# Performance work log

Measured on AMD Instinct MI355X. Metric: run time of the kernel, lower is better.

Reference implementation:

```python
import jax, jax.numpy as jnp
import numpy as np

N = 256          # waveguide_dims
ITERN = 3        # iter_num
B = 8192         # batch
INDEX_END = 10   # MNIST classes
ALPHA = 0.1
G = 0.05 * np.pi
PHI_B = np.pi


def setup_inputs() -> dict:
    key = jax.random.key(0)
    k1, k2, k3, k4, k5 = jax.random.split(key, 5)
    two_pi = 2.0 * np.pi
    return {
        "x_real": jax.random.normal(k1, (B, N), dtype=jnp.float32),
        "x_imag": jax.random.normal(k2, (B, N), dtype=jnp.float32),
        "theta": jax.random.uniform(k3, (ITERN, N, N // 2), dtype=jnp.float32) * two_pi,
        "phi":   jax.random.uniform(k4, (ITERN, N, N // 2), dtype=jnp.float32) * two_pi,
        "gamma": jax.random.uniform(k5, (ITERN, N), dtype=jnp.float32) * two_pi,
    }


def _mzi_mesh(x, theta, phi, gamma):
    """Rectangular (Clements) MZI mesh: N layers of 2x2 rotations + output phases.
    x: [B, N] complex64; theta, phi: [N, N//2]; gamma: [N]."""
    L = theta.shape[0]
    shifts = jnp.arange(L) % 2                      # even/odd layer offset
    full = jnp.ones((N // 2,), dtype=bool)
    odd = full.at[-1].set(False)                    # wrap-around pair inactive on odd layers
    masks = jnp.where((shifts == 1)[:, None], odd[None, :], full[None, :])

    def step(xc, inp):
        th, ph, sh, mk = inp
        xr = jnp.roll(xc, -sh, axis=1).reshape(-1, N // 2, 2)
        x0, x1 = xr[..., 0], xr[..., 1]
        half = 0.5 * th
        s, c = jnp.sin(half), jnp.cos(half)
        pre = 1j * jnp.exp(1j * half)               # common MZI prefactor
        ep = jnp.exp(1j * ph)
        y0 = pre * (ep * s * x0 + c * x1)
        y1 = pre * (ep * c * x0 - s * x1)
        y0 = jnp.where(mk, y0, x0)
        y1 = jnp.where(mk, y1, x1)
        y = jnp.stack([y0, y1], axis=-1).reshape(-1, N)
        return jnp.roll(y, sh, axis=1), None

    x, _ = jax.lax.scan(step, x, (theta, phi, shifts, masks))
    return x * jnp.exp(1j * gamma)[None, :]


def _eo_nonlin(x):
    # phase = 0.5*g*|x|^2 + 0.5*phi_b ; out = sqrt(1-alpha)*cos(phase)*exp(-i phase)*x
    phase = 0.5 * G * (x.real ** 2 + x.imag ** 2) + 0.5 * PHI_B
    return np.float32(np.sqrt(1.0 - ALPHA)) * jnp.cos(phase) * jnp.exp(-1j * phase) * x


def reference(x_real, x_imag, theta, phi, gamma):
    x = x_real.astype(jnp.complex64) + 1j * x_imag.astype(jnp.complex64)
    for i in range(ITERN):
        x = _mzi_mesh(x, theta[i], phi[i], gamma[i])
        if i != ITERN - 1:
            x = _eo_nonlin(x)
    intensity = x.real ** 2 + x.imag ** 2            # cnormsq
    norm = jnp.sqrt(jnp.sum(intensity ** 2, axis=1, keepdims=True))
    intensity = intensity / jnp.maximum(norm, 1e-12)  # F.normalize(dim=1)
    return intensity[:, :INDEX_END]
```

## Files before the change

### kernel.cpp

```cpp
#include <hip/hip_runtime.h>
#include <math.h>

#define NWG 256
#define NPAIR 128
#define NITER 3
#define NBATCH 8192
#define KDIM 512
#define MSZ (512*512)

typedef __attribute__((ext_vector_type(8))) short short8;
typedef __attribute__((ext_vector_type(8))) unsigned short ushort8v;
typedef __attribute__((ext_vector_type(4))) float floatx4;

static __device__ __forceinline__ unsigned short f2bf(float f) {
    unsigned int u = __float_as_uint(f);
    unsigned int r = (u + 0x7fffu + ((u >> 16) & 1u)) >> 16;
    return (unsigned short)r;
}
static __device__ __forceinline__ float bf2f(unsigned short h) {
    return __uint_as_float(((unsigned int)h) << 16);
}
static __device__ __forceinline__ void bsplit(float v, unsigned short &h, unsigned short &l) {
    h = f2bf(v);
    l = f2bf(v - bf2f(h));
}
static __device__ __forceinline__ void async16(const void* g, void* l) {
    __builtin_amdgcn_global_load_lds(
        (const __attribute__((address_space(1))) unsigned int*)g,
        (__attribute__((address_space(3))) unsigned int*)l, 16, 0, 0);
}

static __device__ __forceinline__ void apply2(
    float &x0r, float &x0i, float &x1r, float &x1i,
    const float4 a, const float4 b)
{
    float y0r = a.x*x0r - a.y*x0i + a.z*x1r - a.w*x1i;
    float y0i = a.x*x0i + a.y*x0r + a.z*x1i + a.w*x1r;
    float y1r = b.x*x0r - b.y*x0i + b.z*x1r - b.w*x1i;
    float y1i = b.x*x0i + b.y*x0r + b.z*x1i + b.w*x1r;
    x0r = y0r; x0i = y0i; x1r = y1r; x1i = y1i;
}

__global__ void precompute_kernel(const float* __restrict__ theta,
                                  const float* __restrict__ phi,
                                  const float* __restrict__ gamma,
                                  float* __restrict__ coef,
                                  float* __restrict__ coefT,
                                  float* __restrict__ gexp)
{
    int idx = blockIdx.x * blockDim.x + threadIdx.x;
    if (idx < NITER * NWG * NPAIR) {
        float h  = 0.5f * theta[idx];
        float ph = phi[idx];
        float sh = sinf(h),  ch = cosf(h);
        float sp = sinf(ph), cp = cosf(ph);
        float pr = -sh, pii = ch;
        float qr = pr*cp - pii*sp;
        float qi = pr*sp + pii*cp;
        float Ar = qr*sh,  Ai = qi*sh;
        float Br = pr*ch,  Bi = pii*ch;
        float Cr = qr*ch,  Ci = qi*ch;
        float Dr = -pr*sh, Di = -pii*sh;
        float4* o = (float4*)coef + (size_t)idx * 2;
        o[0] = make_float4(Ar,Ai,Br,Bi);
        o[1] = make_float4(Cr,Ci,Dr,Di);
        float4* ot = (float4*)coefT + (size_t)idx * 2;
        ot[0] = make_float4(Ar,Ai,Cr,Ci);
        ot[1] = make_float4(Br,Bi,Dr,Di);
    }
    if (idx < NITER * NWG) {
        float g = gamma[idx];
        gexp[idx*2]   = cosf(g);
        gexp[idx*2+1] = sinf(g);
    }
}

static __device__ __forceinline__ void store_row(
    unsigned short* __restrict__ bh, unsigned short* __restrict__ bl,
    int row, int lane, bool cj, const float xr[4], const float xi[4])
{
    ushort4 reH, reL, imH, imL, nimH, nimL;
    unsigned short h, l;
#pragma unroll
    for (int e = 0; e < 4; ++e) {
        bsplit(xr[e], h, l);  ((unsigned short*)&reH)[e]  = h; ((unsigned short*)&reL)[e]  = l;
        bsplit(xi[e], h, l);  ((unsigned short*)&imH)[e]  = h; ((unsigned short*)&imL)[e]  = l;
        bsplit(-xi[e], h, l); ((unsigned short*)&nimH)[e] = h; ((unsigned short*)&nimL)[e] = l;
    }
    ushort4 urH = cj ? imH : nimH, urL = cj ? imL : nimL;
    ushort4 llH = cj ? nimH : imH, llL = cj ? nimL : imL;
    *(ushort4*)(bh + (size_t)row*KDIM + 4*lane)             = reH;
    *(ushort4*)(bh + (size_t)row*KDIM + 256 + 4*lane)       = urH;
    *(ushort4*)(bh + (size_t)(row+256)*KDIM + 4*lane)       = llH;
    *(ushort4*)(bh + (size_t)(row+256)*KDIM + 256 + 4*lane) = reH;
    *(ushort4*)(bl + (size_t)row*KDIM + 4*lane)             = reL;
    *(ushort4*)(bl + (size_t)row*KDIM + 256 + 4*lane)       = urL;
    *(ushort4*)(bl + (size_t)(row+256)*KDIM + 4*lane)       = llL;
    *(ushort4*)(bl + (size_t)(row+256)*KDIM + 256 + 4*lane) = reL;
}

static __device__ __forceinline__ void layer_compute2(
    const float4 cc[4], int lane, int sp,
    float ar[4], float ai[4], float br[4], float bi[4])
{
    const float4 c0a = cc[0], c0b = cc[1], c1a = cc[2], c1b = cc[3];
    if ((sp & 1) == 0) {
        apply2(ar[0], ai[0], ar[1], ai[1], c0a, c0b);
        apply2(ar[2], ai[2], ar[3], ai[3], c1a, c1b);
        apply2(br[0], bi[0], br[1], bi[1], c0a, c0b);
        apply2(br[2], bi[2], br[3], bi[3], c1a, c1b);
    } else {
        float tAr = __shfl_down(ar[0], 1, 64);
        float tAi = __shfl_down(ai[0], 1, 64);
        float tBr = __shfl_down(br[0], 1, 64);
        float tBi = __shfl_down(bi[0], 1, 64);
        apply2(ar[1], ai[1], ar[2], ai[2], c0a, c0b);
        apply2(br[1], bi[1], br[2], bi[2], c0a, c0b);
        float x3r = ar[3], x3i = ai[3];
        float y3r = c1a.x*x3r - c1a.y*x3i + c1a.z*tAr - c1a.w*tAi;
        float y3i = c1a.x*x3i + c1a.y*x3r + c1a.z*tAi + c1a.w*tAr;
        float ynr = c1b.x*x3r - c1b.y*x3i + c1b.z*tAr - c1b.w*tAi;
        float yni = c1b.x*x3i + c1b.y*x3r + c1b.z*tAi + c1b.w*tAr;
        float w3r = br[3], w3i = bi[3];
        float z3r = c1a.x*w3r - c1a.y*w3i + c1a.z*tBr - c1a.w*tBi;
        float z3i = c1a.x*w3i + c1a.y*w3r + c1a.z*tBi + c1a.w*tBr;
        float znr = c1b.x*w3r - c1b.y*w3i + c1b.z*tBr - c1b.w*tBi;
        float zni = c1b.x*w3i + c1b.y*w3r + c1b.z*tBi + c1b.w*tBr;
        float rAr = __shfl_up(ynr, 1, 64);
        float rAi = __shfl_up(yni, 1, 64);
        float rBr = __shfl_up(znr, 1, 64);
        float rBi = __shfl_up(zni, 1, 64);
        if (lane != 63) { ar[3] = y3r; ai[3] = y3i; br[3] = z3r; bi[3] = z3i; }
        if (lane != 0)  { ar[0] = rAr; ai[0] = rAi; br[0] = rBr; bi[0] = rBi; }
    }
}

__global__ void propagate_kernel(const float* __restrict__ coef,
                                 const float* __restrict__ coefT,
                                 const float* __restrict__ gexp,
                                 unsigned short* __restrict__ chunkH,
                                 unsigned short* __restrict__ chunkL)
{
    __shared__ __align__(16) char smem[3 * 16384];

    const int tid  = threadIdx.x;
    const int lane = tid & 63;
    const int wv   = tid >> 6;
    const int grp  = blockIdx.x >> 6;
    const int it   = grp >> 2, c = grp & 3;
    const int r0   = (blockIdx.x & 63) * 4 + wv * 2;
    const int r1   = r0 + 1;
    const bool rev = (c & 1);
    const bool cj  = (c == 1) || (c == 2);

    float ar[4], ai[4], br[4], bi[4];
    float gc0 = 1.0f, gs0 = 0.0f, gc1 = 1.0f, gs1 = 0.0f;
    if (c == 3) {
        gc0 = gexp[(it*NWG + r0)*2]; gs0 = gexp[(it*NWG + r0)*2 + 1];
        gc1 = gexp[(it*NWG + r1)*2]; gs1 = gexp[(it*NWG + r1)*2 + 1];
    }
#pragma unroll
    for (int e = 0; e < 4; ++e) {
        bool on0 = (4*lane + e) == r0;
        bool on1 = (4*lane + e) == r1;
        ar[e] = on0 ? gc0 : 0.0f;  ai[e] = on0 ? gs0 : 0.0f;
        br[e] = on1 ? gc1 : 0.0f;  bi[e] = on1 ? gs1 : 0.0f;
    }

    const char* cbb = (const char*)(rev ? coefT : coef)
                    + (size_t)(it*NWG + c*64) * (NPAIR * 32);
    const int slot16 = (tid ^ ((tid >> 3) & 3)) * 16;

    auto stage = [&](int m) {
        char* dst = smem + (m % 3) * 16384;
#pragma unroll
        for (int q = 0; q < 4; ++q) {
            int s = 4*m + q;
            int r = rev ? 63 - s : s;
            const char* srow = cbb + (size_t)r * 4096;
            async16(srow + slot16,        dst + q*4096 + tid*16);
            async16(srow + slot16 + 2048, dst + q*4096 + tid*16 + 2048);
        }
    };

    stage(0); stage(1);

    const int sw = (lane >> 1) & 3;
    for (int m = 0; m < 16; ++m) {
        if (m < 15) asm volatile("s_waitcnt vmcnt(8)" ::: "memory");
        else        asm volatile("s_waitcnt vmcnt(0)" ::: "memory");
        __builtin_amdgcn_s_barrier();
        asm volatile("" ::: "memory");
        if (m < 14) stage(m + 2);
        const char* B = smem + (m % 3) * 16384;

        float4 cc[4][4];
#pragma unroll
        for (int q = 0; q < 4; ++q) {
            const char* Bq = B + q*4096;
            cc[q][0] = *(const float4*)(Bq + 16*(4*lane + (0 ^ sw)));
            cc[q][1] = *(const float4*)(Bq + 16*(4*lane + (1 ^ sw)));
            cc[q][2] = *(const float4*)(Bq + 16*(4*lane + (2 ^ sw)));
            cc[q][3] = *(const float4*)(Bq + 16*(4*lane + (3 ^ sw)));
        }
#pragma unroll
        for (int q = 0; q < 4; ++q) {
            int s = 4*m + q;
            layer_compute2(cc[q], lane, rev ? 63 - s : s, ar, ai, br, bi);
        }
    }

    unsigned short* bh = chunkH + (size_t)grp * MSZ;
    unsigned short* bl = chunkL + (size_t)grp * MSZ;
    store_row(bh, bl, r0, lane, cj, ar, ai);
    store_row(bh, bl, r1, lane, cj, br, bi);
}

__global__ __launch_bounds__(256, 2) void compose_kernel(
    const unsigned short* __restrict__ srcH, const unsigned short* __restrict__ srcL,
    unsigned short* __restrict__ outH, unsigned short* __restrict__ outL,
    unsigned short* __restrict__ bmat, int mode)
{
    __shared__ unsigned short sAh[3][2048], sAl[3][2048], sBh[3][2048], sBl[3][2048];
    const int z = blockIdx.z;
    const unsigned short *Ah, *Al, *Bh, *Bl;
    if (mode == 0) {
        int it = z >> 1, wh = z & 1;
        int ai = it*4 + (wh ? 3 : 0), bi = it*4 + (wh ? 2 : 1);
        Ah = srcH + (size_t)ai*MSZ; Al = srcL + (size_t)ai*MSZ;
        Bh = srcH + (size_t)bi*MSZ; Bl = srcL + (size_t)bi*MSZ;
    } else {
        Ah = srcH + (size_t)(2*z+1)*MSZ; Al = srcL + (size_t)(2*z+1)*MSZ;
        Bh = srcH + (size_t)(2*z)*MSZ;   Bl = srcL + (size_t)(2*z)*MSZ;
    }
    const int tid = threadIdx.x, lane = tid & 63, wv = tid >> 6;
    const int quad = lane >> 4, l16 = lane & 15;
    const int m0 = blockIdx.x * 64, n0 = blockIdx.y * 64;
    const unsigned short* src = (wv==0)?Ah:(wv==1)?Al:(wv==2)?Bh:Bl;
    unsigned short (*dstb)[2048] = (wv==0)?sAh:(wv==1)?sAl:(wv==2)?sBh:sBl;
    const int r0 = (wv < 2) ? m0 : n0;
    const int trowb = lane >> 2, tcol = (lane & 3) * 8;

    const unsigned short* sp[4];
#pragma unroll
    for (int i = 0; i < 4; ++i)
        sp[i] = src + (size_t)(r0 + i*16 + trowb)*KDIM + tcol;

    auto stage = [&](int s) {
        int kt = s * 32, bs = s % 3;
#pragma unroll
        for (int i = 0; i < 4; ++i)
            async16(sp[i] + kt, &dstb[bs][i*512 + lane*8]);
    };
    stage(0); stage(1);

    floatx4 acc[4] = {};
    for (int s = 0; s < 16; ++s) {
        if (s < 15) asm volatile("s_waitcnt vmcnt(4)" ::: "memory");
        else        asm volatile("s_waitcnt vmcnt(0)" ::: "memory");
        __builtin_amdgcn_s_barrier();
        asm volatile("" ::: "memory");
        if (s < 14) stage(s + 2);
        const int bs = s % 3;
        short8 ah = *(const short8*)&sAh[bs][(16*wv + l16)*32 + quad*8];
        short8 al = *(const short8*)&sAl[bs][(16*wv + l16)*32 + quad*8];
#pragma unroll
        for (int ni = 0; ni < 4; ++ni) {
            short8 bh = *(const short8*)&sBh[bs][(16*ni + l16)*32 + quad*8];
            short8 bl = *(const short8*)&sBl[bs][(16*ni + l16)*32 + quad*8];
            acc[ni] = __builtin_amdgcn_mfma_f32_16x16x32_bf16(ah, bh, acc[ni], 0,0,0);
            acc[ni] = __builtin_amdgcn_mfma_f32_16x16x32_bf16(ah, bl, acc[ni], 0,0,0);
            acc[ni] = __builtin_amdgcn_mfma_f32_16x16x32_bf16(al, bh, acc[ni], 0,0,0);
        }
    }
#pragma unroll
    for (int ni = 0; ni < 4; ++ni)
#pragma unroll
        for (int rg = 0; rg < 4; ++rg) {
            int r = m0 + 16*wv + quad*4 + rg;
            int cc = n0 + 16*ni + l16;
            float v = acc[ni][rg];
            if (mode == 0) {
                float vs = (((z & 1) == 0) && ((r >= 256) != (cc >= 256))) ? -v : v;
                unsigned short h, l; bsplit(vs, h, l);
                outH[(size_t)z*MSZ + (size_t)r*KDIM + cc] = h;
                outL[(size_t)z*MSZ + (size_t)r*KDIM + cc] = l;
            } else {
                bmat[(size_t)z*MSZ + (size_t)r*KDIM + cc] = f2bf(v);
            }
        }
}

__global__ void convert_kernel(const float* __restrict__ xre,
                               const float* __restrict__ xim,
                               unsigned short* __restrict__ xb)
{
    int idx = blockIdx.x * 256 + threadIdx.x;
    int b = idx >> 5, j = (idx & 31) << 3;
    const float* rp = xre + (size_t)b * 256 + j;
    const float* ip = xim + (size_t)b * 256 + j;
    float4 r0 = *(const float4*)rp, r1 = *(const float4*)(rp + 4);
    float4 i0 = *(const float4*)ip, i1 = *(const float4*)(ip + 4);
    ushort8v re, im;
    re[0]=f2bf(r0.x); re[1]=f2bf(r0.y); re[2]=f2bf(r0.z); re[3]=f2bf(r0.w);
    re[4]=f2bf(r1.x); re[5]=f2bf(r1.y); re[6]=f2bf(r1.z); re[7]=f2bf(r1.w);
    im[0]=f2bf(i0.x); im[1]=f2bf(i0.y); im[2]=f2bf(i0.z); im[3]=f2bf(i0.w);
    im[4]=f2bf(i1.x); im[5]=f2bf(i1.y); im[6]=f2bf(i1.z); im[7]=f2bf(i1.w);
    *(ushort8v*)(xb + (size_t)b * KDIM + j)       = re;
    *(ushort8v*)(xb + (size_t)b * KDIM + 256 + j) = im;
}

__global__ __launch_bounds__(256, 2) void gemm_kernel(
    const unsigned short* __restrict__ A, const unsigned short* __restrict__ Bm,
    int mode, unsigned short* __restrict__ xout, float* __restrict__ Iout)
{
    __shared__ unsigned short sA[3][64*32];
    __shared__ unsigned short sB[3][128*32];
    const int tid = threadIdx.x, lane = tid & 63, wv = tid >> 6;
    const int quad = lane >> 4, l16 = lane & 15;
    const int m0 = blockIdx.x * 64, n0 = blockIdx.y * 64;
    const int trowb = lane >> 2, tcol = (lane & 3) * 8;

    const unsigned short* srcA = A + (size_t)(m0 + 16*wv + trowb)*KDIM + tcol;
    int trow0 = 32*wv + trowb,  trow1 = 32*wv + 16 + trowb;
    int grow0 = (trow0 < 64) ? (n0 + trow0) : (n0 + trow0 + 192);
    int grow1 = (trow1 < 64) ? (n0 + trow1) : (n0 + trow1 + 192);
    const unsigned short* srcB0 = Bm + (size_t)grow0*KDIM + tcol;
    const unsigned short* srcB1 = Bm + (size_t)grow1*KDIM + tcol;

    auto stage = [&](int s) {
        int kt = s * 32, bs = s % 3;
        async16(srcA  + kt, &sA[bs][wv*512 + lane*8]);
        async16(srcB0 + kt, &sB[bs][(32*wv)*32 + lane*8]);
        async16(srcB1 + kt, &sB[bs][(32*wv + 16)*32 + lane*8]);
    };
    stage(0); stage(1);

    floatx4 acc[8] = {};
    for (int s = 0; s < 16; ++s) {
        if (s < 15) asm volatile("s_waitcnt vmcnt(3)" ::: "memory");
        else        asm volatile("s_waitcnt vmcnt(0)" ::: "memory");
        __builtin_amdgcn_s_barrier();
        asm volatile("" ::: "memory");
        if (s < 14) stage(s + 2);
        const int bs = s % 3;
        short8 a = *(const short8*)&sA[bs][(16*wv + l16)*32 + quad*8];
#pragma unroll
        for (int ni = 0; ni < 8; ++ni) {
            short8 b = *(const short8*)&sB[bs][(16*ni + l16)*32 + quad*8];
            acc[ni] = __builtin_amdgcn_mfma_f32_16x16x32_bf16(a, b, acc[ni], 0,0,0);
        }
    }
#pragma unroll
    for (int ni = 0; ni < 4; ++ni)
#pragma unroll
        for (int rg = 0; rg < 4; ++rg) {
            int row = m0 + 16*wv + quad*4 + rg;
            int cc  = n0 + 16*ni + l16;
            float yr = acc[ni][rg], yi = acc[ni+4][rg];
            if (mode == 2) {
                Iout[(size_t)row*256 + cc] = yr*yr + yi*yi;
            } else {
                float I = yr*yr + yi*yi;
                float phase = 0.078539816339744831f * I + 1.5707963267948966f;
                float sp, cp; __sincosf(phase, &sp, &cp);
                float f = 0.94868329805051381f * cp;
                xout[(size_t)row*KDIM + cc]       = f2bf(f*(cp*yr + sp*yi));
                xout[(size_t)row*KDIM + cc + 256] = f2bf(f*(cp*yi - sp*yr));
            }
        }
}

__global__ void final_kernel(const float* __restrict__ Ibuf,
                             float* __restrict__ out)
{
    const int lane = threadIdx.x & 63;
    const int wv   = threadIdx.x >> 6;
    const int row  = blockIdx.x * 4 + wv;
    float4 v = *(const float4*)(Ibuf + (size_t)row * 256 + 4*lane);
    float ss = v.x*v.x + v.y*v.y + v.z*v.z + v.w*v.w;
#pragma unroll
    for (int d = 1; d < 64; d <<= 1) ss += __shfl_xor(ss, d, 64);
    float inv = 1.0f / fmaxf(sqrtf(ss), 1e-12f);
    float* o = out + (size_t)row * 10;
    if (lane == 0)      { o[0]=v.x*inv; o[1]=v.y*inv; o[2]=v.z*inv; o[3]=v.w*inv; }
    else if (lane == 1) { o[4]=v.x*inv; o[5]=v.y*inv; o[6]=v.z*inv; o[7]=v.w*inv; }
    else if (lane == 2) { o[8]=v.x*inv; o[9]=v.y*inv; }
}

extern "C" void kernel_launch(void* const* d_in, const int* in_sizes, int n_in,
                              void* d_out, int out_size, void* d_ws, size_t ws_size,
                              hipStream_t stream)
{
    const float* x_real = (const float*)d_in[0];
    const float* x_imag = (const float*)d_in[1];
    const float* theta  = (const float*)d_in[2];
    const float* phi    = (const float*)d_in[3];
    const float* gamma  = (const float*)d_in[4];

    char* ws = (char*)d_ws;
    float* coef  = (float*)(ws + 0);
    float* coefT = (float*)(ws + 3145728);
    float* gexp  = (float*)(ws + 6291456);
    unsigned short* chunkH = (unsigned short*)(ws + 6297600);
    unsigned short* chunkL = (unsigned short*)(ws + 12589056);
    unsigned short* PH   = (unsigned short*)(ws + 0);
    unsigned short* PL   = (unsigned short*)(ws + 3145728);
    unsigned short* xbuf0 = (unsigned short*)(ws + 6297600);
    unsigned short* xbuf1 = (unsigned short*)(ws + 14686208);
    float* Ibuf = (float*)(ws + 14686208);
    unsigned short* Bmat = (unsigned short*)(ws + 23074816);

    precompute_kernel<<<(NITER*NWG*NPAIR + 255)/256, 256, 0, stream>>>(
        theta, phi, gamma, coef, coefT, gexp);

    propagate_kernel<<<768, 128, 0, stream>>>(coef, coefT, gexp, chunkH, chunkL);

    compose_kernel<<<dim3(8,8,6), 256, 0, stream>>>(chunkH, chunkL, PH, PL, Bmat, 0);
    compose_kernel<<<dim3(8,8,3), 256, 0, stream>>>(PH, PL, PH, PL, Bmat, 1);

    convert_kernel<<<NBATCH*NWG/8/256, 256, 0, stream>>>(x_real, x_imag, xbuf0);

    gemm_kernel<<<dim3(128,4), 256, 0, stream>>>(xbuf0, Bmat,           0, xbuf1, (float*)nullptr);
    gemm_kernel<<<dim3(128,4), 256, 0, stream>>>(xbuf1, Bmat + MSZ,     1, xbuf0, (float*)nullptr);
    gemm_kernel<<<dim3(128,4), 256, 0, stream>>>(xbuf0, Bmat + 2*MSZ,   2, (unsigned short*)nullptr, Ibuf);

    final_kernel<<<NBATCH/4, 256, 0, stream>>>(Ibuf, (float*)d_out);
}
```

Measured before the change: 169.2 us.

## Fuse fp32-to-bf16 input conversion into first GEMM and deepen K-stage

Removes the separate convert kernel: the first GEMM now loads fp32 real/imag inputs directly into registers, converts them to bf16 and writes them to shared memory in a 3-deep software pipeline. The other GEMM modes now stage 64-wide K tiles (two 32-wide halves) per barrier, halving barrier count. This doubles shared memory per block, which may lower occupancy, and the register-staged A path adds conversion work inside the GEMM.

```diff
diff --git a/kernel.cpp b/kernel.cpp
--- a/kernel.cpp
+++ b/kernel.cpp
@@ -291,66 +291,97 @@
         }
 }
 
-__global__ void convert_kernel(const float* __restrict__ xre,
-                               const float* __restrict__ xim,
-                               unsigned short* __restrict__ xb)
-{
-    int idx = blockIdx.x * 256 + threadIdx.x;
-    int b = idx >> 5, j = (idx & 31) << 3;
-    const float* rp = xre + (size_t)b * 256 + j;
-    const float* ip = xim + (size_t)b * 256 + j;
-    float4 r0 = *(const float4*)rp, r1 = *(const float4*)(rp + 4);
-    float4 i0 = *(const float4*)ip, i1 = *(const float4*)(ip + 4);
-    ushort8v re, im;
-    re[0]=f2bf(r0.x); re[1]=f2bf(r0.y); re[2]=f2bf(r0.z); re[3]=f2bf(r0.w);
-    re[4]=f2bf(r1.x); re[5]=f2bf(r1.y); re[6]=f2bf(r1.z); re[7]=f2bf(r1.w);
-    im[0]=f2bf(i0.x); im[1]=f2bf(i0.y); im[2]=f2bf(i0.z); im[3]=f2bf(i0.w);
-    im[4]=f2bf(i1.x); im[5]=f2bf(i1.y); im[6]=f2bf(i1.z); im[7]=f2bf(i1.w);
-    *(ushort8v*)(xb + (size_t)b * KDIM + j)       = re;
-    *(ushort8v*)(xb + (size_t)b * KDIM + 256 + j) = im;
-}
-
 __global__ __launch_bounds__(256, 2) void gemm_kernel(
     const unsigned short* __restrict__ A, const unsigned short* __restrict__ Bm,
-    int mode, unsigned short* __restrict__ xout, float* __restrict__ Iout)
-{
-    __shared__ unsigned short sA[3][64*32];
-    __shared__ unsigned short sB[3][128*32];
+    int mode, const float* __restrict__ xre, const float* __restrict__ xim,
+    unsigned short* __restrict__ xout, float* __restrict__ Iout)
+{
+    __shared__ unsigned short sA[3][2][64*32];
+    __shared__ unsigned short sB[3][2][128*32];
     const int tid = threadIdx.x, lane = tid & 63, wv = tid >> 6;
     const int quad = lane >> 4, l16 = lane & 15;
     const int m0 = blockIdx.x * 64, n0 = blockIdx.y * 64;
     const int trowb = lane >> 2, tcol = (lane & 3) * 8;
 
-    const unsigned short* srcA = A + (size_t)(m0 + 16*wv + trowb)*KDIM + tcol;
+    const int arow = m0 + 16*wv + trowb;
     int trow0 = 32*wv + trowb,  trow1 = 32*wv + 16 + trowb;
     int grow0 = (trow0 < 64) ? (n0 + trow0) : (n0 + trow0 + 192);
     int grow1 = (trow1 < 64) ? (n0 + trow1) : (n0 + trow1 + 192);
     const unsigned short* srcB0 = Bm + (size_t)grow0*KDIM + tcol;
     const unsigned short* srcB1 = Bm + (size_t)grow1*KDIM + tcol;
 
-    auto stage = [&](int s) {
-        int kt = s * 32, bs = s % 3;
-        async16(srcA  + kt, &sA[bs][wv*512 + lane*8]);
-        async16(srcB0 + kt, &sB[bs][(32*wv)*32 + lane*8]);
-        async16(srcB1 + kt, &sB[bs][(32*wv + 16)*32 + lane*8]);
-    };
-    stage(0); stage(1);
-
     floatx4 acc[8] = {};
-    for (int s = 0; s < 16; ++s) {
-        if (s < 15) asm volatile("s_waitcnt vmcnt(3)" ::: "memory");
-        else        asm volatile("s_waitcnt vmcnt(0)" ::: "memory");
-        __builtin_amdgcn_s_barrier();
-        asm volatile("" ::: "memory");
-        if (s < 14) stage(s + 2);
-        const int bs = s % 3;
-        short8 a = *(const short8*)&sA[bs][(16*wv + l16)*32 + quad*8];
-#pragma unroll
-        for (int ni = 0; ni < 8; ++ni) {
-            short8 b = *(const short8*)&sB[bs][(16*ni + l16)*32 + quad*8];
-            acc[ni] = __builtin_amdgcn_mfma_f32_16x16x32_bf16(a, b, acc[ni], 0,0,0);
-        }
-    }
+
+    if (mode == 0) {
+        float4 areg[3][2];
+        auto loadA = [&](int t, float4 arg[2]) {
+            const float* srcx = (t < 8) ? xre : xim;
+            const float* p = srcx + (size_t)arow * 256 + ((t*32) & 255) + tcol;
+            arg[0] = *(const float4*)p;
+            arg[1] = *(const float4*)(p + 4);
+        };
+        auto stageB = [&](int t) {
+            int kt = t * 32, bs = t % 3;
+            async16(srcB0 + kt, &sB[bs][0][(32*wv)*32 + lane*8]);
+            async16(srcB1 + kt, &sB[bs][0][(32*wv + 16)*32 + lane*8]);
+        };
+        auto writeA = [&](int t, const float4 arg[2]) {
+            ushort8v v;
+            v[0]=f2bf(arg[0].x); v[1]=f2bf(arg[0].y); v[2]=f2bf(arg[0].z); v[3]=f2bf(arg[0].w);
+            v[4]=f2bf(arg[1].x); v[5]=f2bf(arg[1].y); v[6]=f2bf(arg[1].z); v[7]=f2bf(arg[1].w);
+            *(ushort8v*)&sA[t % 3][0][wv*512 + lane*8] = v;
+        };
+        loadA(0, areg[0]); loadA(1, areg[1]); loadA(2, areg[2]);
+        stageB(0); stageB(1);
+        asm volatile("s_waitcnt vmcnt(6)" ::: "memory");
+        writeA(0, areg[0]); writeA(1, areg[1]);
+#pragma unroll
+        for (int i = 0; i < 16; ++i) {
+            if (i < 15) asm volatile("s_waitcnt vmcnt(2) lgkmcnt(0)" ::: "memory");
+            else        asm volatile("s_waitcnt vmcnt(0) lgkmcnt(0)" ::: "memory");
+            __builtin_amdgcn_s_barrier();
+            asm volatile("" ::: "memory");
+            if (i + 3 <= 15) loadA(i + 3, areg[(i + 3) % 3]);
+            if (i + 2 <= 15) { stageB(i + 2); writeA(i + 2, areg[(i + 2) % 3]); }
+            const int bs = i % 3;
+            short8 a = *(const short8*)&sA[bs][0][(16*wv + l16)*32 + quad*8];
+#pragma unroll
+            for (int ni = 0; ni < 8; ++ni) {
+                short8 b = *(const short8*)&sB[bs][0][(16*ni + l16)*32 + quad*8];
+                acc[ni] = __builtin_amdgcn_mfma_f32_16x16x32_bf16(a, b, acc[ni], 0,0,0);
+            }
+        }
+    } else {
+        const unsigned short* srcA = A + (size_t)arow*KDIM + tcol;
+        auto stage = [&](int s) {
+            int kt = s * 64, bs = s % 3;
+            async16(srcA  + kt,      &sA[bs][0][wv*512 + lane*8]);
+            async16(srcA  + kt + 32, &sA[bs][1][wv*512 + lane*8]);
+            async16(srcB0 + kt,      &sB[bs][0][(32*wv)*32 + lane*8]);
+            async16(srcB0 + kt + 32, &sB[bs][1][(32*wv)*32 + lane*8]);
+            async16(srcB1 + kt,      &sB[bs][0][(32*wv + 16)*32 + lane*8]);
+            async16(srcB1 + kt + 32, &sB[bs][1][(32*wv + 16)*32 + lane*8]);
+        };
+        stage(0); stage(1);
+        for (int s = 0; s < 8; ++s) {
+            if (s < 7) asm volatile("s_waitcnt vmcnt(6)" ::: "memory");
+            else       asm volatile("s_waitcnt vmcnt(0)" ::: "memory");
+            __builtin_amdgcn_s_barrier();
+            asm volatile("" ::: "memory");
+            if (s < 6) stage(s + 2);
+            const int bs = s % 3;
+#pragma unroll
+            for (int h = 0; h < 2; ++h) {
+                short8 a = *(const short8*)&sA[bs][h][(16*wv + l16)*32 + quad*8];
+#pragma unroll
+                for (int ni = 0; ni < 8; ++ni) {
+                    short8 b = *(const short8*)&sB[bs][h][(16*ni + l16)*32 + quad*8];
+                    acc[ni] = __builtin_amdgcn_mfma_f32_16x16x32_bf16(a, b, acc[ni], 0,0,0);
+                }
+            }
+        }
+    }
+
 #pragma unroll
     for (int ni = 0; ni < 4; ++ni)
 #pragma unroll
@@ -419,11 +450,9 @@
     compose_kernel<<<dim3(8,8,6), 256, 0, stream>>>(chunkH, chunkL, PH, PL, Bmat, 0);
     compose_kernel<<<dim3(8,8,3), 256, 0, stream>>>(PH, PL, PH, PL, Bmat, 1);
 
-    convert_kernel<<<NBATCH*NWG/8/256, 256, 0, stream>>>(x_real, x_imag, xbuf0);
-
-    gemm_kernel<<<dim3(128,4), 256, 0, stream>>>(xbuf0, Bmat,           0, xbuf1, (float*)nullptr);
-    gemm_kernel<<<dim3(128,4), 256, 0, stream>>>(xbuf1, Bmat + MSZ,     1, xbuf0, (float*)nullptr);
-    gemm_kernel<<<dim3(128,4), 256, 0, stream>>>(xbuf0, Bmat + 2*MSZ,   2, (unsigned short*)nullptr, Ibuf);
+    gemm_kernel<<<dim3(128,4), 256, 0, stream>>>(nullptr, Bmat,         0, x_real, x_imag, xbuf1, (float*)nullptr);
+    gemm_kernel<<<dim3(128,4), 256, 0, stream>>>(xbuf1,   Bmat + MSZ,   1, nullptr, nullptr, xbuf0, (float*)nullptr);
+    gemm_kernel<<<dim3(128,4), 256, 0, stream>>>(xbuf0,   Bmat + 2*MSZ, 2, nullptr, nullptr, (unsigned short*)nullptr, Ibuf);
 
     final_kernel<<<NBATCH/4, 256, 0, stream>>>(Ibuf, (float*)d_out);
 }
```

Result: faster. 164.3 us (-2.9%).

## Fuse convert, three GEMMs, nonlinearity and normalize into one persistent tail kernel

Applied to the files above, without the earlier changes.

Replaces the convert kernel, the three per-iteration GEMM launches and the final normalize kernel with a single kernel. Each block keeps 32 batch rows resident in swizzled LDS across all three 512x512 transfer matrices and applies the EO nonlinearity in place between stages. This removes the global round trips of the intermediate activations and several launches. In exchange it uses 128KB of LDS with one 512-thread block per CU and only 256 blocks, and every block re-streams all three B matrices from L2.

```diff
diff --git a/kernel.cpp b/kernel.cpp
--- a/kernel.cpp
+++ b/kernel.cpp
@@ -291,101 +291,163 @@
         }
 }
 
-__global__ void convert_kernel(const float* __restrict__ xre,
-                               const float* __restrict__ xim,
-                               unsigned short* __restrict__ xb)
-{
-    int idx = blockIdx.x * 256 + threadIdx.x;
-    int b = idx >> 5, j = (idx & 31) << 3;
-    const float* rp = xre + (size_t)b * 256 + j;
-    const float* ip = xim + (size_t)b * 256 + j;
-    float4 r0 = *(const float4*)rp, r1 = *(const float4*)(rp + 4);
-    float4 i0 = *(const float4*)ip, i1 = *(const float4*)(ip + 4);
-    ushort8v re, im;
-    re[0]=f2bf(r0.x); re[1]=f2bf(r0.y); re[2]=f2bf(r0.z); re[3]=f2bf(r0.w);
-    re[4]=f2bf(r1.x); re[5]=f2bf(r1.y); re[6]=f2bf(r1.z); re[7]=f2bf(r1.w);
-    im[0]=f2bf(i0.x); im[1]=f2bf(i0.y); im[2]=f2bf(i0.z); im[3]=f2bf(i0.w);
-    im[4]=f2bf(i1.x); im[5]=f2bf(i1.y); im[6]=f2bf(i1.z); im[7]=f2bf(i1.w);
-    *(ushort8v*)(xb + (size_t)b * KDIM + j)       = re;
-    *(ushort8v*)(xb + (size_t)b * KDIM + 256 + j) = im;
-}
-
-__global__ __launch_bounds__(256, 2) void gemm_kernel(
-    const unsigned short* __restrict__ A, const unsigned short* __restrict__ Bm,
-    int mode, unsigned short* __restrict__ xout, float* __restrict__ Iout)
-{
-    __shared__ unsigned short sA[3][64*32];
-    __shared__ unsigned short sB[3][128*32];
+__global__ __launch_bounds__(512, 1) void fused_tail_kernel(
+    const unsigned short* __restrict__ Bmat,
+    const float* __restrict__ xre, const float* __restrict__ xim,
+    float* __restrict__ out)
+{
+    __shared__ __align__(16) char lds[131072];
     const int tid = threadIdx.x, lane = tid & 63, wv = tid >> 6;
     const int quad = lane >> 4, l16 = lane & 15;
-    const int m0 = blockIdx.x * 64, n0 = blockIdx.y * 64;
-    const int trowb = lane >> 2, tcol = (lane & 3) * 8;
-
-    const unsigned short* srcA = A + (size_t)(m0 + 16*wv + trowb)*KDIM + tcol;
-    int trow0 = 32*wv + trowb,  trow1 = 32*wv + 16 + trowb;
-    int grow0 = (trow0 < 64) ? (n0 + trow0) : (n0 + trow0 + 192);
-    int grow1 = (trow1 < 64) ? (n0 + trow1) : (n0 + trow1 + 192);
-    const unsigned short* srcB0 = Bm + (size_t)grow0*KDIM + tcol;
-    const unsigned short* srcB1 = Bm + (size_t)grow1*KDIM + tcol;
-
-    auto stage = [&](int s) {
-        int kt = s * 32, bs = s % 3;
-        async16(srcA  + kt, &sA[bs][wv*512 + lane*8]);
-        async16(srcB0 + kt, &sB[bs][(32*wv)*32 + lane*8]);
-        async16(srcB1 + kt, &sB[bs][(32*wv + 16)*32 + lane*8]);
+    const int rbase = blockIdx.x * 32;
+    const int nb = 32 * wv;
+
+    auto sx = [&](int row, int colByte) -> char* {
+        return lds + 98304 + row*1024 + (colByte ^ ((row & 7) << 4));
     };
-    stage(0); stage(1);
-
-    floatx4 acc[8] = {};
-    for (int s = 0; s < 16; ++s) {
-        if (s < 15) asm volatile("s_waitcnt vmcnt(3)" ::: "memory");
+
+    {
+        float4 v0[4], v1[4]; int xr_[4], xc_[4];
+#pragma unroll
+        for (int c = 0; c < 4; ++c) {
+            int k = tid + c*512;
+            int row = k >> 6, rem = k & 63, half = rem >> 5, j8 = (rem & 31) << 3;
+            const float* s = (half ? xim : xre) + ((size_t)(rbase + row))*256 + j8;
+            v0[c] = *(const float4*)s; v1[c] = *(const float4*)(s + 4);
+            xr_[c] = row; xc_[c] = (half*256 + j8)*2;
+        }
+        asm volatile("s_waitcnt vmcnt(0)" ::: "memory");
+#pragma unroll
+        for (int c = 0; c < 4; ++c) {
+            ushort8v u;
+            u[0]=f2bf(v0[c].x); u[1]=f2bf(v0[c].y); u[2]=f2bf(v0[c].z); u[3]=f2bf(v0[c].w);
+            u[4]=f2bf(v1[c].x); u[5]=f2bf(v1[c].y); u[6]=f2bf(v1[c].z); u[7]=f2bf(v1[c].w);
+            *(ushort8v*)sx(xr_[c], xc_[c]) = u;
+        }
+    }
+
+    auto stageB = [&](int t) {
+        const unsigned short* src = Bmat + ((size_t)(t >> 4))*MSZ + (size_t)(t & 15)*32;
+        char* dst = lds + (t % 3)*32768;
+#pragma unroll
+        for (int c = 0; c < 4; ++c) {
+            int slot = tid + c*512, r = slot >> 2, q = slot & 3;
+            async16(src + (size_t)r*KDIM + q*8, dst + slot*16);
+        }
+    };
+    stageB(0); stageB(1);
+    asm volatile("s_waitcnt lgkmcnt(0)" ::: "memory");
+
+    floatx4 accr[2][2] = {}, acci[2][2] = {};
+
+    for (int t = 0; t < 48; ++t) {
+        if (t < 46) asm volatile("s_waitcnt vmcnt(4)" ::: "memory");
         else        asm volatile("s_waitcnt vmcnt(0)" ::: "memory");
         __builtin_amdgcn_s_barrier();
         asm volatile("" ::: "memory");
-        if (s < 14) stage(s + 2);
-        const int bs = s % 3;
-        short8 a = *(const short8*)&sA[bs][(16*wv + l16)*32 + quad*8];
-#pragma unroll
-        for (int ni = 0; ni < 8; ++ni) {
-            short8 b = *(const short8*)&sB[bs][(16*ni + l16)*32 + quad*8];
-            acc[ni] = __builtin_amdgcn_mfma_f32_16x16x32_bf16(a, b, acc[ni], 0,0,0);
-        }
-    }
-#pragma unroll
-    for (int ni = 0; ni < 4; ++ni)
+        if (t < 46) stageB(t + 2);
+
+        if (t == 16 || t == 32) {
+#pragma unroll
+            for (int f = 0; f < 2; ++f)
+#pragma unroll
+            for (int nl = 0; nl < 2; ++nl)
+#pragma unroll
+            for (int rg = 0; rg < 4; ++rg) {
+                float yr = accr[f][nl][rg], yi = acci[f][nl][rg];
+                float I = yr*yr + yi*yi;
+                float ph = 0.078539816339744831f * I + 1.5707963267948966f;
+                float sp, cp; __sincosf(ph, &sp, &cp);
+                float fm = 0.94868329805051381f * cp;
+                int row = 16*f + quad*4 + rg;
+                int col = nb + 16*nl + l16;
+                *(unsigned short*)sx(row, col*2)       = f2bf(fm*(cp*yr + sp*yi));
+                *(unsigned short*)sx(row, col*2 + 512) = f2bf(fm*(cp*yi - sp*yr));
+            }
+            asm volatile("s_waitcnt lgkmcnt(0)" ::: "memory");
+            __builtin_amdgcn_s_barrier();
+            asm volatile("" ::: "memory");
+#pragma unroll
+            for (int f = 0; f < 2; ++f)
+#pragma unroll
+            for (int nl = 0; nl < 2; ++nl) {
+                accr[f][nl] = (floatx4){0.f,0.f,0.f,0.f};
+                acci[f][nl] = (floatx4){0.f,0.f,0.f,0.f};
+            }
+        }
+
+        const int kB = (t & 15) * 64;
+        const char* Bb = lds + (t % 3)*32768;
+        short8 a0 = *(const short8*)sx(l16,      kB + quad*16);
+        short8 a1 = *(const short8*)sx(16 + l16, kB + quad*16);
+        short8 br0 = *(const short8*)(Bb + (nb + l16)*64 + quad*16);
+        short8 br1 = *(const short8*)(Bb + (nb + 16 + l16)*64 + quad*16);
+        short8 bi0 = *(const short8*)(Bb + (256 + nb + l16)*64 + quad*16);
+        short8 bi1 = *(const short8*)(Bb + (256 + nb + 16 + l16)*64 + quad*16);
+        accr[0][0] = __builtin_amdgcn_mfma_f32_16x16x32_bf16(a0, br0, accr[0][0], 0,0,0);
+        accr[0][1] = __builtin_amdgcn_mfma_f32_16x16x32_bf16(a0, br1, accr[0][1], 0,0,0);
+        accr[1][0] = __builtin_amdgcn_mfma_f32_16x16x32_bf16(a1, br0, accr[1][0], 0,0,0);
+        accr[1][1] = __builtin_amdgcn_mfma_f32_16x16x32_bf16(a1, br1, accr[1][1], 0,0,0);
+        acci[0][0] = __builtin_amdgcn_mfma_f32_16x16x32_bf16(a0, bi0, acci[0][0], 0,0,0);
+        acci[0][1] = __builtin_amdgcn_mfma_f32_16x16x32_bf16(a0, bi1, acci[0][1], 0,0,0);
+        acci[1][0] = __builtin_amdgcn_mfma_f32_16x16x32_bf16(a1, bi0, acci[1][0], 0,0,0);
+        acci[1][1] = __builtin_amdgcn_mfma_f32_16x16x32_bf16(a1, bi1, acci[1][1], 0,0,0);
+    }
+
+    float I[2][2][4];
+    float p[2][4];
+#pragma unroll
+    for (int f = 0; f < 2; ++f)
+#pragma unroll
+    for (int rg = 0; rg < 4; ++rg) {
+        float s = 0.0f;
+#pragma unroll
+        for (int nl = 0; nl < 2; ++nl) {
+            float yr = accr[f][nl][rg], yi = acci[f][nl][rg];
+            float Iv = yr*yr + yi*yi;
+            I[f][nl][rg] = Iv;
+            s += Iv*Iv;
+        }
+        p[f][rg] = s;
+    }
+#pragma unroll
+    for (int d = 1; d < 16; d <<= 1) {
+#pragma unroll
+        for (int f = 0; f < 2; ++f)
+#pragma unroll
+        for (int rg = 0; rg < 4; ++rg)
+            p[f][rg] += __shfl_xor(p[f][rg], d, 64);
+    }
+    float* scr = (float*)lds;
+    if (l16 == 0) {
+#pragma unroll
+        for (int f = 0; f < 2; ++f)
+#pragma unroll
+        for (int rg = 0; rg < 4; ++rg)
+            scr[wv*32 + 16*f + quad*4 + rg] = p[f][rg];
+    }
+    asm volatile("s_waitcnt lgkmcnt(0)" ::: "memory");
+    __builtin_amdgcn_s_barrier();
+    asm volatile("" ::: "memory");
+    float* invb = (float*)(lds + 2048);
+    if (tid < 32) {
+        float s = 0.0f;
+#pragma unroll
+        for (int w = 0; w < 8; ++w) s += scr[w*32 + tid];
+        invb[tid] = 1.0f / fmaxf(sqrtf(s), 1e-12f);
+    }
+    asm volatile("s_waitcnt lgkmcnt(0)" ::: "memory");
+    __builtin_amdgcn_s_barrier();
+    asm volatile("" ::: "memory");
+    if (wv == 0 && l16 < 10) {
+#pragma unroll
+        for (int f = 0; f < 2; ++f)
 #pragma unroll
         for (int rg = 0; rg < 4; ++rg) {
-            int row = m0 + 16*wv + quad*4 + rg;
-            int cc  = n0 + 16*ni + l16;
-            float yr = acc[ni][rg], yi = acc[ni+4][rg];
-            if (mode == 2) {
-                Iout[(size_t)row*256 + cc] = yr*yr + yi*yi;
-            } else {
-                float I = yr*yr + yi*yi;
-                float phase = 0.078539816339744831f * I + 1.5707963267948966f;
-                float sp, cp; __sincosf(phase, &sp, &cp);
-                float f = 0.94868329805051381f * cp;
-                xout[(size_t)row*KDIM + cc]       = f2bf(f*(cp*yr + sp*yi));
-                xout[(size_t)row*KDIM + cc + 256] = f2bf(f*(cp*yi - sp*yr));
-            }
-        }
-}
-
-__global__ void final_kernel(const float* __restrict__ Ibuf,
-                             float* __restrict__ out)
-{
-    const int lane = threadIdx.x & 63;
-    const int wv   = threadIdx.x >> 6;
-    const int row  = blockIdx.x * 4 + wv;
-    float4 v = *(const float4*)(Ibuf + (size_t)row * 256 + 4*lane);
-    float ss = v.x*v.x + v.y*v.y + v.z*v.z + v.w*v.w;
-#pragma unroll
-    for (int d = 1; d < 64; d <<= 1) ss += __shfl_xor(ss, d, 64);
-    float inv = 1.0f / fmaxf(sqrtf(ss), 1e-12f);
-    float* o = out + (size_t)row * 10;
-    if (lane == 0)      { o[0]=v.x*inv; o[1]=v.y*inv; o[2]=v.z*inv; o[3]=v.w*inv; }
-    else if (lane == 1) { o[4]=v.x*inv; o[5]=v.y*inv; o[6]=v.z*inv; o[7]=v.w*inv; }
-    else if (lane == 2) { o[8]=v.x*inv; o[9]=v.y*inv; }
+            int row = 16*f + quad*4 + rg;
+            out[((size_t)(rbase + row))*10 + l16] = I[f][0][rg] * invb[row];
+        }
+    }
 }
 
 extern "C" void kernel_launch(void* const* d_in, const int* in_sizes, int n_in,
@@ -406,9 +468,6 @@
     unsigned short* chunkL = (unsigned short*)(ws + 12589056);
     unsigned short* PH   = (unsigned short*)(ws + 0);
     unsigned short* PL   = (unsigned short*)(ws + 3145728);
-    unsigned short* xbuf0 = (unsigned short*)(ws + 6297600);
-    unsigned short* xbuf1 = (unsigned short*)(ws + 14686208);
-    float* Ibuf = (float*)(ws + 14686208);
     unsigned short* Bmat = (unsigned short*)(ws + 23074816);
 
     precompute_kernel<<<(NITER*NWG*NPAIR + 255)/256, 256, 0, stream>>>(
@@ -419,11 +478,5 @@
     compose_kernel<<<dim3(8,8,6), 256, 0, stream>>>(chunkH, chunkL, PH, PL, Bmat, 0);
     compose_kernel<<<dim3(8,8,3), 256, 0, stream>>>(PH, PL, PH, PL, Bmat, 1);
 
-    convert_kernel<<<NBATCH*NWG/8/256, 256, 0, stream>>>(x_real, x_imag, xbuf0);
-
-    gemm_kernel<<<dim3(128,4), 256, 0, stream>>>(xbuf0, Bmat,           0, xbuf1, (float*)nullptr);
-    gemm_kernel<<<dim3(128,4), 256, 0, stream>>>(xbuf1, Bmat + MSZ,     1, xbuf0, (float*)nullptr);
-    gemm_kernel<<<dim3(128,4), 256, 0, stream>>>(xbuf0, Bmat + 2*MSZ,   2, (unsigned short*)nullptr, Ibuf);
-
-    final_kernel<<<NBATCH/4, 256, 0, stream>>>(Ibuf, (float*)d_out);
-}
+    fused_tail_kernel<<<256, 512, 0, stream>>>(Bmat, x_real, x_imag, (float*)d_out);
+}
```

Result: faster. 157.5 us (median of 2 runs) (-6.9%).
